# Kernel tuning notes

Hardware: AMD Instinct MI355X
Metric: run time of the kernel (lower is better)

The kernel has to match this reference:

```python
import jax, jax.numpy as jnp
import numpy as np

H, W = 4096, 4096
KH, KW = 15, 15


def setup_inputs() -> dict:
    key = jax.random.key(0)
    k1, k2 = jax.random.split(key)
    X = jax.random.normal(k1, (H, W), dtype=jnp.float32)
    weight = jax.random.uniform(k2, (KH, KW), dtype=jnp.float32)
    bias = jnp.zeros((1,), dtype=jnp.float32)
    return {"X": X, "weight": weight, "bias": bias}


def reference(X, weight, bias):
    # 2D cross-correlation, 'valid' padding: out[i,j] = sum(X[i:i+kh, j:j+kw] * K) + b
    lhs = X[None, None, :, :]                 # [1,1,H,W]
    rhs = weight[None, None, :, :]            # [1,1,KH,KW] (cross-correlation: no flip)
    out = jax.lax.conv_general_dilated(
        lhs, rhs,
        window_strides=(1, 1),
        padding="VALID",
        dimension_numbers=("NCHW", "OIHW", "NCHW"),
    )[0, 0]                                   # [H-KH+1, W-KW+1]
    return out + bias[0]
```

## Files before the change

### kernel.cpp

```cpp
#include <hip/hip_runtime.h>
#include <hip/hip_bf16.h>


#define IN_DIM   4096
#define OUT_DIM  4082
#define KDIM     15
#define BM       128
#define BN       96
#define NTX      6
#define SLAB_R   142
#define SLAB_CE  120
#define SLAB_CB  240
#define SLAB_CH  15

typedef __attribute__((ext_vector_type(8))) short  short8;
typedef __attribute__((ext_vector_type(4))) float  f32x4;

__global__ __launch_bounds__(256, 3) void conv15_mfma(
    const float* __restrict__ X, const float* __restrict__ Wt,
    const float* __restrict__ bias, float* __restrict__ out) {
  __shared__ __align__(16) unsigned short sX[SLAB_R * SLAB_CE];
  __shared__ __align__(16) unsigned short sB[KDIM * 16 * 32];

  const int tid = threadIdx.x;
  const int x0 = blockIdx.x * BN;
  const int y0 = blockIdx.y * BM;

  for (int idx = tid; idx < KDIM * 512; idx += 256) {
    const int ky = idx >> 9;
    const int n  = (idx >> 5) & 15;
    const int k  = idx & 31;
    const int kx = k - n;
    unsigned short v = 0;
    if (kx >= 0 && kx < KDIM) {
      __hip_bfloat16 h = __float2bfloat16(Wt[ky * KDIM + kx]);
      v = *reinterpret_cast<const unsigned short*>(&h);
    }
    sB[idx] = v;
  }

  for (int idx = tid; idx < SLAB_R * SLAB_CH; idx += 256) {
    const int r = idx / SLAB_CH;
    const int c = idx - r * SLAB_CH;
    int gr = y0 + r;           if (gr > IN_DIM - 1) gr = IN_DIM - 1;
    int gc = x0 + c * 8;       if (gc > IN_DIM - 8) gc = IN_DIM - 8;
    const float* p = X + (size_t)gr * IN_DIM + gc;
    const f32x4 a = *reinterpret_cast<const f32x4*>(p);
    const f32x4 b = *reinterpret_cast<const f32x4*>(p + 4);
    float f[8] = {a.x, a.y, a.z, a.w, b.x, b.y, b.z, b.w};
    short8 pk;
#pragma unroll
    for (int j = 0; j < 8; ++j) {
      __hip_bfloat16 h = __float2bfloat16(f[j]);
      pk[j] = *reinterpret_cast<const short*>(&h);
    }
    *reinterpret_cast<short8*>(
        reinterpret_cast<char*>(sX) + r * SLAB_CB + c * 16) = pk;
  }
  __syncthreads();

  const int lane = tid & 63;
  const int wv   = tid >> 6;
  const int m    = lane & 15;
  const int g    = lane >> 4;

  short8 bf[KDIM];
#pragma unroll
  for (int ky = 0; ky < KDIM; ++ky)
    bf[ky] = *reinterpret_cast<const short8*>(
        reinterpret_cast<const char*>(sB) + ky * 1024 + m * 64 + g * 16);

  f32x4 acc[2][NTX];
#pragma unroll
  for (int a = 0; a < 2; ++a)
#pragma unroll
    for (int b = 0; b < NTX; ++b)
      acc[a][b] = (f32x4){0.f, 0.f, 0.f, 0.f};

  const char* base0 = reinterpret_cast<const char*>(sX)
                    + (32 * wv + m) * SLAB_CB + 16 * g;
  const char* base1 = base0 + 16 * SLAB_CB;

#pragma unroll
  for (int ky = 0; ky < KDIM; ++ky) {
#pragma unroll
    for (int xt = 0; xt < NTX; ++xt) {
      const short8 a0 = *reinterpret_cast<const short8*>(
          base0 + ky * SLAB_CB + 32 * xt);
      acc[0][xt] = __builtin_amdgcn_mfma_f32_16x16x32_bf16(
          a0, bf[ky], acc[0][xt], 0, 0, 0);
    }
#pragma unroll
    for (int xt = 0; xt < NTX; ++xt) {
      const short8 a1 = *reinterpret_cast<const short8*>(
          base1 + ky * SLAB_CB + 32 * xt);
      acc[1][xt] = __builtin_amdgcn_mfma_f32_16x16x32_bf16(
          a1, bf[ky], acc[1][xt], 0, 0, 0);
    }
  }

  const float bv = bias[0];
#pragma unroll
  for (int ty = 0; ty < 2; ++ty) {
    const int gy0 = y0 + (2 * wv + ty) * 16 + g * 4;
#pragma unroll
    for (int xt = 0; xt < NTX; ++xt) {
      const int ox = x0 + xt * 16 + m;
      if (ox < OUT_DIM) {
#pragma unroll
        for (int q = 0; q < 4; ++q) {
          const int oy = gy0 + q;
          if (oy < OUT_DIM)
            out[(size_t)oy * OUT_DIM + ox] = acc[ty][xt][q] + bv;
        }
      }
    }
  }
}

extern "C" void kernel_launch(void* const* d_in, const int* in_sizes, int n_in,
                              void* d_out, int out_size, void* d_ws, size_t ws_size,
                              hipStream_t stream) {
  const float* X    = (const float*)d_in[0];
  const float* Wt   = (const float*)d_in[1];
  const float* bias = (const float*)d_in[2];
  float* out = (float*)d_out;

  dim3 grid((OUT_DIM + BN - 1) / BN,
            (OUT_DIM + BM - 1) / BM);
  conv15_mfma<<<grid, 256, 0, stream>>>(X, Wt, bias, out);
}
```

Before: 142.1 us.

## Shrink tile width, build banded weights in registers, remap blocks across XCDs

Narrows the output tile from 96 to 80 columns and raises launch bounds to 4 waves per SIMD, trading more halo overhead for higher occupancy. The banded Toeplitz weight matrix is no longer staged in LDS; each lane builds its B fragments from a compact 15x15 weight table, which cuts LDS use and setup work. A 1D grid with an XCD-aware block remap groups neighbouring tiles on the same XCD for L2 reuse. Bias is folded into the accumulator init. The risks are more redundant halo loads and per-lane select logic in setup.

```diff
diff --git a/kernel.cpp b/kernel.cpp
--- a/kernel.cpp
+++ b/kernel.cpp
@@ -6,37 +6,38 @@
 #define OUT_DIM  4082
 #define KDIM     15
 #define BM       128
-#define BN       96
-#define NTX      6
+#define BN       80
+#define NTX      5
 #define SLAB_R   142
-#define SLAB_CE  120
-#define SLAB_CB  240
-#define SLAB_CH  15
+#define SLAB_CE  96
+#define SLAB_CB  192
+#define SLAB_CH  12
+#define GRID_X   52
+#define GRID_Y   32
+#define NWG      (GRID_X * GRID_Y)
+#define CPX      (NWG / 8)
 
 typedef __attribute__((ext_vector_type(8))) short  short8;
 typedef __attribute__((ext_vector_type(4))) float  f32x4;
 
-__global__ __launch_bounds__(256, 3) void conv15_mfma(
+__global__ __launch_bounds__(256, 4) void conv15_mfma(
     const float* __restrict__ X, const float* __restrict__ Wt,
     const float* __restrict__ bias, float* __restrict__ out) {
   __shared__ __align__(16) unsigned short sX[SLAB_R * SLAB_CE];
-  __shared__ __align__(16) unsigned short sB[KDIM * 16 * 32];
+  __shared__ __align__(16) unsigned short sW[KDIM * KDIM];
 
   const int tid = threadIdx.x;
-  const int x0 = blockIdx.x * BN;
-  const int y0 = blockIdx.y * BM;
 
-  for (int idx = tid; idx < KDIM * 512; idx += 256) {
-    const int ky = idx >> 9;
-    const int n  = (idx >> 5) & 15;
-    const int k  = idx & 31;
-    const int kx = k - n;
-    unsigned short v = 0;
-    if (kx >= 0 && kx < KDIM) {
-      __hip_bfloat16 h = __float2bfloat16(Wt[ky * KDIM + kx]);
-      v = *reinterpret_cast<const unsigned short*>(&h);
-    }
-    sB[idx] = v;
+  const int bid = blockIdx.x;
+  const int lin = (bid & 7) * CPX + (bid >> 3);
+  const int bx  = lin % GRID_X;
+  const int by  = lin / GRID_X;
+  const int x0 = bx * BN;
+  const int y0 = by * BM;
+
+  if (tid < KDIM * KDIM) {
+    __hip_bfloat16 h = __float2bfloat16(Wt[tid]);
+    sW[tid] = *reinterpret_cast<const unsigned short*>(&h);
   }
 
   for (int idx = tid; idx < SLAB_R * SLAB_CH; idx += 256) {
@@ -66,16 +67,25 @@
 
   short8 bf[KDIM];
 #pragma unroll
-  for (int ky = 0; ky < KDIM; ++ky)
-    bf[ky] = *reinterpret_cast<const short8*>(
-        reinterpret_cast<const char*>(sB) + ky * 1024 + m * 64 + g * 16);
+  for (int ky = 0; ky < KDIM; ++ky) {
+    short8 t;
+#pragma unroll
+    for (int j = 0; j < 8; ++j) {
+      const int kx = g * 8 + j - m;
+      const int cl = kx < 0 ? 0 : (kx > 14 ? 14 : kx);
+      const unsigned short v = sW[ky * KDIM + cl];
+      t[j] = (kx >= 0 && kx <= 14) ? (short)v : (short)0;
+    }
+    bf[ky] = t;
+  }
 
+  const float bv = bias[0];
   f32x4 acc[2][NTX];
 #pragma unroll
   for (int a = 0; a < 2; ++a)
 #pragma unroll
     for (int b = 0; b < NTX; ++b)
-      acc[a][b] = (f32x4){0.f, 0.f, 0.f, 0.f};
+      acc[a][b] = (f32x4){bv, bv, bv, bv};
 
   const char* base0 = reinterpret_cast<const char*>(sX)
                     + (32 * wv + m) * SLAB_CB + 16 * g;
@@ -99,7 +109,6 @@
     }
   }
 
-  const float bv = bias[0];
 #pragma unroll
   for (int ty = 0; ty < 2; ++ty) {
     const int gy0 = y0 + (2 * wv + ty) * 16 + g * 4;
@@ -111,7 +120,7 @@
         for (int q = 0; q < 4; ++q) {
           const int oy = gy0 + q;
           if (oy < OUT_DIM)
-            out[(size_t)oy * OUT_DIM + ox] = acc[ty][xt][q] + bv;
+            out[(size_t)oy * OUT_DIM + ox] = acc[ty][xt][q];
         }
       }
     }
@@ -126,7 +135,5 @@
   const float* bias = (const float*)d_in[2];
   float* out = (float*)d_out;
 
-  dim3 grid((OUT_DIM + BN - 1) / BN,
-            (OUT_DIM + BM - 1) / BM);
-  conv15_mfma<<<grid, 256, 0, stream>>>(X, Wt, bias, out);
+  conv15_mfma<<<NWG, 256, 0, stream>>>(X, Wt, bias, out);
 }
```

New measurement: 129.8 us. 8.7% less time.
